# Performance work log

Measured on AMD Instinct MI355X. Metric: run time of the kernel, lower is better.

The kernel has to match this reference:

```python
import jax, jax.numpy as jnp
import numpy as np

B, E, H, W, L = 16, 32, 512, 512, 3  # batch, emb channels, height, width, n classes (bg/plant/disease)
MAX_NEIGHBOR = 3


def _per_image_loss(emb, pred, label, neighbor):
    """emb: (E,H,W) f32; pred: (L,H,W) f32 logits; label: (H,W) int32; neighbor: (L,MAX_NEIGHBOR) int32."""
    P = H * W
    emb_f = emb.reshape(E, P)                                      # (E,P)
    lab_f = label.reshape(P)
    onehot = (lab_f[None, :] == jnp.arange(L)[:, None]).astype(emb.dtype)  # (L,P)
    counts = onehot.sum(axis=1)                                    # (L,)

    # per-label mean embeddings (segment mean) and L2-normalized means (F.normalize eps=1e-12)
    means = (onehot @ emb_f.T) / counts[:, None]                   # (L,E)
    norm_means = means / jnp.maximum(jnp.linalg.norm(means, axis=1, keepdims=True), 1e-12)

    # intra loss: mean over masked pixels of (1 - cos(norm_mean, pixel)), labels 1..L-1
    pix_hat = emb_f / jnp.maximum(jnp.linalg.norm(emb_f, axis=0, keepdims=True), 1e-8)  # CosineSimilarity eps
    cos = norm_means @ pix_hat                                     # (L,P)
    intra_per = (onehot * (1.0 - cos)).sum(axis=1) / counts        # (L,)
    intra = intra_per[1:].sum() / (L - 1)

    # inter loss: pairwise cosine of normalized means, masked by neighbor table
    S = norm_means @ norm_means.T                                  # (L,L)
    # inter_mask: for main_label>=1, mark neighbor entries until first 0 (break semantics)
    valid = jnp.cumprod((neighbor != 0).astype(jnp.float32), axis=1)        # (L,MAX_NEIGHBOR)
    rows = jnp.broadcast_to(jnp.arange(L)[:, None], (L, MAX_NEIGHBOR))
    row_ok = (rows >= 1).astype(jnp.float32)
    mask = jnp.zeros((L, L), dtype=jnp.float32).at[
        rows.reshape(-1), neighbor.reshape(-1)
    ].max((valid * row_ok).reshape(-1))
    inter = (S * mask).sum() / mask.sum()

    # cross-entropy (labels in [0,L), ignore_index=255 never hit here), mean over pixels
    logp = jax.nn.log_softmax(pred, axis=0)                        # (L,H,W)
    ce = -jnp.take_along_axis(logp, label[None, :, :].astype(jnp.int32), axis=0).mean()

    return intra + inter + ce


def setup_inputs() -> dict:
    key = jax.random.key(0)
    k1, k2, k3 = jax.random.split(key, 3)
    embedding = jax.random.normal(k1, (B, E, H, W), dtype=jnp.float32)
    prediction = jax.random.normal(k2, (B, L, H, W), dtype=jnp.float32)
    class_label = jax.random.randint(k3, (B, H, W), 0, L).astype(jnp.int32)
    # realistic neighbor table: plant(1)<->disease(2) adjacent, 0 = terminator
    nb = np.tile(np.array([[0, 0, 0], [2, 0, 0], [1, 0, 0]], dtype=np.int32), (B, 1, 1))
    neighbor = jnp.asarray(nb)
    return {"embedding": embedding, "prediction": prediction,
            "class_label": class_label, "neighbor": neighbor}


def reference(embedding, prediction, class_label, neighbor):
    losses = jax.vmap(_per_image_loss)(embedding, prediction, class_label, neighbor)  # (B,)
    return losses.sum()
```

## Files before the change

kernel.cpp:

```cpp
#include <hip/hip_runtime.h>
#include <math.h>

#define BATCH 16
#define EMB   32
#define HW    262144
#define NL    3

#define BLOCKS_PER_IMG 128
#define PX_PER_BLOCK   (HW / BLOCKS_PER_IMG)
#define WAVES_PER_BLK  4
#define PX_PER_WAVE    (PX_PER_BLOCK / WAVES_PER_BLK)
#define TILE_PX        32
#define N_ITERS        (PX_PER_WAVE / TILE_PX)

#define WS_COUNTS 0
#define WS_SE     64
#define WS_SH     (WS_SE + BATCH*96)
#define WS_CE     (WS_SH + BATCH*96)
#define WS_FLOATS (WS_CE + 1)

__device__ __forceinline__ float ce1(float a, float b, float c, int l) {
    const float m = fmaxf(fmaxf(a, b), c);
    const float s = __expf(a - m) + __expf(b - m) + __expf(c - m);
    const float zl = (l == 0) ? a : ((l == 1) ? b : c);
    return m + __logf(s) - zl;
}

__global__ __launch_bounds__(256) void fused_kernel(
        const float* __restrict__ emb, const float* __restrict__ pred,
        const int* __restrict__ label, float* __restrict__ ws)
{
    const int tid  = threadIdx.x;
    const int lane = tid & 63;
    const int wv   = tid >> 6;
    const int ps   = lane & 7;
    const int cg   = lane >> 3;
    const int b    = blockIdx.x / BLOCKS_PER_IMG;
    const int blk  = blockIdx.x % BLOCKS_PER_IMG;

    const float* embB  = emb   + (size_t)b * EMB * HW;
    const float* predB = pred  + (size_t)b * 3 * HW;
    const int*   labB  = label + (size_t)b * HW;

    const size_t base = (size_t)blk * PX_PER_BLOCK
                      + (size_t)wv * PX_PER_WAVE
                      + (size_t)ps * 4;

    const float* ch0 = embB + (size_t)(cg*4+0)*HW + base;
    const float* ch1 = embB + (size_t)(cg*4+1)*HW + base;
    const float* ch2 = embB + (size_t)(cg*4+2)*HW + base;
    const float* ch3 = embB + (size_t)(cg*4+3)*HW + base;
    const int*   lb  = labB + base;
    const float* pr  = predB + base;

    float accE[NL][4] = {};
    float accH[2][4]  = {};
    float cnt0 = 0.f, cnt1 = 0.f, cnt2 = 0.f;
    float ce = 0.f;

    for (int it = 0; it < N_ITERS; ++it) {
        const size_t off = (size_t)it * TILE_PX;

        const float4 v0 = *(const float4*)(ch0 + off);
        const float4 v1 = *(const float4*)(ch1 + off);
        const float4 v2 = *(const float4*)(ch2 + off);
        const float4 v3 = *(const float4*)(ch3 + off);
        const int4  lab = *(const int4*)(lb + off);

        const bool doCE = (cg == (it & 7));
        float4 z0, z1, z2;
        if (doCE) {
            z0 = *(const float4*)(pr + off);
            z1 = *(const float4*)(pr + HW + off);
            z2 = *(const float4*)(pr + 2*HW + off);
        }

        float4 s;
        s.x = v0.x*v0.x + v1.x*v1.x + v2.x*v2.x + v3.x*v3.x;
        s.y = v0.y*v0.y + v1.y*v1.y + v2.y*v2.y + v3.y*v3.y;
        s.z = v0.z*v0.z + v1.z*v1.z + v2.z*v2.z + v3.z*v3.z;
        s.w = v0.w*v0.w + v1.w*v1.w + v2.w*v2.w + v3.w*v3.w;
        s.x += __shfl_xor(s.x, 8);  s.x += __shfl_xor(s.x, 16);  s.x += __shfl_xor(s.x, 32);
        s.y += __shfl_xor(s.y, 8);  s.y += __shfl_xor(s.y, 16);  s.y += __shfl_xor(s.y, 32);
        s.z += __shfl_xor(s.z, 8);  s.z += __shfl_xor(s.z, 16);  s.z += __shfl_xor(s.z, 32);
        s.w += __shfl_xor(s.w, 8);  s.w += __shfl_xor(s.w, 16);  s.w += __shfl_xor(s.w, 32);

        float invn[4];
        invn[0] = 1.0f / fmaxf(sqrtf(s.x), 1e-8f);
        invn[1] = 1.0f / fmaxf(sqrtf(s.y), 1e-8f);
        invn[2] = 1.0f / fmaxf(sqrtf(s.z), 1e-8f);
        invn[3] = 1.0f / fmaxf(sqrtf(s.w), 1e-8f);

        const float chv[4][4] = {
            {v0.x, v1.x, v2.x, v3.x},
            {v0.y, v1.y, v2.y, v3.y},
            {v0.z, v1.z, v2.z, v3.z},
            {v0.w, v1.w, v2.w, v3.w}};
        const int labs[4] = {lab.x, lab.y, lab.z, lab.w};

        #pragma unroll
        for (int j = 0; j < 4; ++j) {
            const float m0 = (labs[j] == 0) ? 1.f : 0.f;
            const float m1 = (labs[j] == 1) ? 1.f : 0.f;
            const float m2 = (labs[j] == 2) ? 1.f : 0.f;
            const float iv = invn[j];
            if (cg == 0) { cnt0 += m0; cnt1 += m1; cnt2 += m2; }
            #pragma unroll
            for (int k = 0; k < 4; ++k) {
                const float v  = chv[j][k];
                const float vh = v * iv;
                accE[0][k] = fmaf(m0, v,  accE[0][k]);
                accE[1][k] = fmaf(m1, v,  accE[1][k]);
                accE[2][k] = fmaf(m2, v,  accE[2][k]);
                accH[0][k] = fmaf(m1, vh, accH[0][k]);
                accH[1][k] = fmaf(m2, vh, accH[1][k]);
            }
        }

        if (doCE) {
            ce += ce1(z0.x, z1.x, z2.x, labs[0]);
            ce += ce1(z0.y, z1.y, z2.y, labs[1]);
            ce += ce1(z0.z, z1.z, z2.z, labs[2]);
            ce += ce1(z0.w, z1.w, z2.w, labs[3]);
        }
    }

    #pragma unroll
    for (int o = 4; o >= 1; o >>= 1) {
        #pragma unroll
        for (int l = 0; l < NL; ++l)
            #pragma unroll
            for (int k = 0; k < 4; ++k)
                accE[l][k] += __shfl_xor(accE[l][k], o);
        #pragma unroll
        for (int l = 0; l < 2; ++l)
            #pragma unroll
            for (int k = 0; k < 4; ++k)
                accH[l][k] += __shfl_xor(accH[l][k], o);
        cnt0 += __shfl_xor(cnt0, o);
        cnt1 += __shfl_xor(cnt1, o);
        cnt2 += __shfl_xor(cnt2, o);
    }
    #pragma unroll
    for (int o = 32; o >= 1; o >>= 1) ce += __shfl_xor(ce, o);

    if (ps == 0) {
        float* se = ws + WS_SE + b * 96;
        float* sh = ws + WS_SH + b * 96;
        #pragma unroll
        for (int l = 0; l < NL; ++l)
            #pragma unroll
            for (int k = 0; k < 4; ++k)
                atomicAdd(&se[l*32 + cg*4 + k], accE[l][k]);
        #pragma unroll
        for (int l = 0; l < 2; ++l)
            #pragma unroll
            for (int k = 0; k < 4; ++k)
                atomicAdd(&sh[(l+1)*32 + cg*4 + k], accH[l][k]);
    }
    if (lane == 0) {
        atomicAdd(&ws[WS_CE], ce * (1.0f / (float)HW));
        atomicAdd(&ws[WS_COUNTS + b*4 + 0], cnt0);
        atomicAdd(&ws[WS_COUNTS + b*4 + 1], cnt1);
        atomicAdd(&ws[WS_COUNTS + b*4 + 2], cnt2);
    }
}

__global__ __launch_bounds__(512) void final_kernel(
        const int* __restrict__ nbr, const float* __restrict__ ws,
        float* __restrict__ out)
{
    const int tid = threadIdx.x;
    const int b = tid >> 5;
    const int e = tid & 31;
    __shared__ float total;
    if (tid == 0) total = 0.f;
    __syncthreads();

    const float* se = ws + WS_SE + b * 96;
    const float* sh = ws + WS_SH + b * 96;
    const float c0 = ws[WS_COUNTS + b*4 + 0];
    const float c1 = ws[WS_COUNTS + b*4 + 1];
    const float c2 = ws[WS_COUNTS + b*4 + 2];

    float mean0 = se[0*32 + e] / c0;
    float mean1 = se[1*32 + e] / c1;
    float mean2 = se[2*32 + e] / c2;

    float n0 = mean0*mean0, n1 = mean1*mean1, n2 = mean2*mean2;
    #pragma unroll
    for (int o = 16; o >= 1; o >>= 1) {
        n0 += __shfl_xor(n0, o);
        n1 += __shfl_xor(n1, o);
        n2 += __shfl_xor(n2, o);
    }
    const float nm0 = mean0 / fmaxf(sqrtf(n0), 1e-12f);
    const float nm1 = mean1 / fmaxf(sqrtf(n1), 1e-12f);
    const float nm2 = mean2 / fmaxf(sqrtf(n2), 1e-12f);

    float d1  = nm1 * sh[1*32 + e];
    float d2  = nm2 * sh[2*32 + e];
    float s10 = nm1 * nm0, s11 = nm1 * nm1, s12 = nm1 * nm2;
    float s20 = nm2 * nm0, s21 = nm2 * nm1, s22 = nm2 * nm2;
    #pragma unroll
    for (int o = 16; o >= 1; o >>= 1) {
        d1  += __shfl_xor(d1, o);  d2  += __shfl_xor(d2, o);
        s10 += __shfl_xor(s10, o); s11 += __shfl_xor(s11, o); s12 += __shfl_xor(s12, o);
        s20 += __shfl_xor(s20, o); s21 += __shfl_xor(s21, o); s22 += __shfl_xor(s22, o);
    }

    if (e == 0) {
        float S[3][3];
        S[1][0] = s10; S[1][1] = s11; S[1][2] = s12;
        S[2][0] = s20; S[2][1] = s21; S[2][2] = s22;
        S[0][0] = S[0][1] = S[0][2] = 0.f;
        float mask[3][3] = {{0.f,0.f,0.f},{0.f,0.f,0.f},{0.f,0.f,0.f}};
        for (int row = 1; row < 3; ++row) {
            int prod = 1;
            for (int j = 0; j < 3; ++j) {
                const int v = nbr[b*9 + row*3 + j];
                if (v == 0) prod = 0;
                if (prod) mask[row][v] = 1.f;
            }
        }
        float num = 0.f, den = 0.f;
        for (int row = 1; row < 3; ++row)
            for (int col = 0; col < 3; ++col) {
                num += S[row][col] * mask[row][col];
                den += mask[row][col];
            }
        const float inter = num / den;
        const float ip1 = 1.f - d1 / c1;
        const float ip2 = 1.f - d2 / c2;
        const float loss = 0.5f * (ip1 + ip2) + inter;
        atomicAdd(&total, loss);
    }
    __syncthreads();
    if (tid == 0) out[0] = total + ws[WS_CE];
}

extern "C" void kernel_launch(void* const* d_in, const int* in_sizes, int n_in,
                              void* d_out, int out_size, void* d_ws, size_t ws_size,
                              hipStream_t stream) {
    const float* emb   = (const float*)d_in[0];
    const float* pred  = (const float*)d_in[1];
    const int*   label = (const int*)d_in[2];
    const int*   nbr   = (const int*)d_in[3];
    float* ws  = (float*)d_ws;
    float* out = (float*)d_out;

    hipMemsetAsync(d_ws, 0, WS_FLOATS * sizeof(float), stream);
    fused_kernel<<<BATCH * BLOCKS_PER_IMG, 256, 0, stream>>>(emb, pred, label, ws);
    final_kernel<<<1, 512, 0, stream>>>(nbr, ws, out);
}
```

Baseline: 864.7 us.

## Stage embedding tiles in LDS, one 256-pixel tile per block

Replaces the per-wave streaming loop with one 256-pixel tile per block. The block loads all 32 channels into a padded shared-memory tile and computes pixel norms through a shared partial-sum buffer. The transposed tile is then reduced per channel group, which removes the per-pixel cross-lane shuffles for norms and spreads the cross-entropy work evenly across threads. The cost is eight times more blocks and roughly twice as many global atomics onto the same few per-image addresses. The float4 stores into rows with an odd stride of 257 floats may also be misaligned.

```diff
diff --git a/kernel.cpp b/kernel.cpp
--- a/kernel.cpp
+++ b/kernel.cpp
@@ -6,12 +6,8 @@
 #define HW    262144
 #define NL    3
 
-#define BLOCKS_PER_IMG 128
-#define PX_PER_BLOCK   (HW / BLOCKS_PER_IMG)
-#define WAVES_PER_BLK  4
-#define PX_PER_WAVE    (PX_PER_BLOCK / WAVES_PER_BLK)
-#define TILE_PX        32
-#define N_ITERS        (PX_PER_WAVE / TILE_PX)
+#define TILE_PX        256
+#define TILES_PER_IMG  (HW / TILE_PX)
 
 #define WS_COUNTS 0
 #define WS_SE     64
@@ -30,113 +26,90 @@
         const float* __restrict__ emb, const float* __restrict__ pred,
         const int* __restrict__ label, float* __restrict__ ws)
 {
-    const int tid  = threadIdx.x;
-    const int lane = tid & 63;
-    const int wv   = tid >> 6;
-    const int ps   = lane & 7;
-    const int cg   = lane >> 3;
-    const int b    = blockIdx.x / BLOCKS_PER_IMG;
-    const int blk  = blockIdx.x % BLOCKS_PER_IMG;
-
-    const float* embB  = emb   + (size_t)b * EMB * HW;
-    const float* predB = pred  + (size_t)b * 3 * HW;
-    const int*   labB  = label + (size_t)b * HW;
-
-    const size_t base = (size_t)blk * PX_PER_BLOCK
-                      + (size_t)wv * PX_PER_WAVE
-                      + (size_t)ps * 4;
-
-    const float* ch0 = embB + (size_t)(cg*4+0)*HW + base;
-    const float* ch1 = embB + (size_t)(cg*4+1)*HW + base;
-    const float* ch2 = embB + (size_t)(cg*4+2)*HW + base;
-    const float* ch3 = embB + (size_t)(cg*4+3)*HW + base;
-    const int*   lb  = labB + base;
-    const float* pr  = predB + base;
+    const int tid = threadIdx.x;
+    const int wv  = tid >> 6;
+    const int l   = tid & 63;
+    const int b   = blockIdx.x >> 10;
+    const int t0  = (blockIdx.x & 1023) * TILE_PX;
+
+    const float* embB  = emb   + (size_t)b * EMB * HW + t0;
+    const float* predB = pred  + (size_t)b * 3 * HW + t0;
+    const int*   labB  = label + (size_t)b * HW + t0;
+
+    __shared__ float embT[32][TILE_PX + 1];
+    __shared__ float partF[4][TILE_PX];
+    __shared__ float invnL[TILE_PX];
+    __shared__ int   labL[TILE_PX];
+
+    float4 ps4 = {0.f, 0.f, 0.f, 0.f};
+    #pragma unroll
+    for (int i = 0; i < 8; ++i) {
+        const int c = wv * 8 + i;
+        const float4 v = *(const float4*)(embB + (size_t)c * HW + l * 4);
+        ps4.x = fmaf(v.x, v.x, ps4.x);
+        ps4.y = fmaf(v.y, v.y, ps4.y);
+        ps4.z = fmaf(v.z, v.z, ps4.z);
+        ps4.w = fmaf(v.w, v.w, ps4.w);
+        *(float4*)&embT[c][l * 4] = v;
+    }
+    *(float4*)&partF[wv][l * 4] = ps4;
+    if (wv == 0) {
+        const int4 lb4 = *(const int4*)(labB + l * 4);
+        *(int4*)&labL[l * 4] = lb4;
+    }
+    __syncthreads();
+
+    const float ss = partF[0][tid] + partF[1][tid] + partF[2][tid] + partF[3][tid];
+    const float iv = 1.0f / fmaxf(sqrtf(ss), 1e-8f);
+    invnL[tid] = iv;
+    const int lbp = labL[tid];
+    const float z0 = predB[tid];
+    const float z1 = predB[HW + tid];
+    const float z2 = predB[2 * HW + tid];
+    float ce = ce1(z0, z1, z2, lbp);
+    __syncthreads();
+
+    const int cg = tid >> 5;
+    const int pl = tid & 31;
+    const int c0 = cg * 4;
 
     float accE[NL][4] = {};
     float accH[2][4]  = {};
     float cnt0 = 0.f, cnt1 = 0.f, cnt2 = 0.f;
-    float ce = 0.f;
-
-    for (int it = 0; it < N_ITERS; ++it) {
-        const size_t off = (size_t)it * TILE_PX;
-
-        const float4 v0 = *(const float4*)(ch0 + off);
-        const float4 v1 = *(const float4*)(ch1 + off);
-        const float4 v2 = *(const float4*)(ch2 + off);
-        const float4 v3 = *(const float4*)(ch3 + off);
-        const int4  lab = *(const int4*)(lb + off);
-
-        const bool doCE = (cg == (it & 7));
-        float4 z0, z1, z2;
-        if (doCE) {
-            z0 = *(const float4*)(pr + off);
-            z1 = *(const float4*)(pr + HW + off);
-            z2 = *(const float4*)(pr + 2*HW + off);
+
+    #pragma unroll
+    for (int s = 0; s < 8; ++s) {
+        const int p = pl + 32 * s;
+        const int lb = labL[p];
+        const float ivp = invnL[p];
+        const float m0 = (lb == 0) ? 1.f : 0.f;
+        const float m1 = (lb == 1) ? 1.f : 0.f;
+        const float m2 = (lb == 2) ? 1.f : 0.f;
+        if (cg == 0) { cnt0 += m0; cnt1 += m1; cnt2 += m2; }
+        #pragma unroll
+        for (int k = 0; k < 4; ++k) {
+            const float v  = embT[c0 + k][p];
+            const float vh = v * ivp;
+            accE[0][k] = fmaf(m0, v,  accE[0][k]);
+            accE[1][k] = fmaf(m1, v,  accE[1][k]);
+            accE[2][k] = fmaf(m2, v,  accE[2][k]);
+            accH[0][k] = fmaf(m1, vh, accH[0][k]);
+            accH[1][k] = fmaf(m2, vh, accH[1][k]);
         }
-
-        float4 s;
-        s.x = v0.x*v0.x + v1.x*v1.x + v2.x*v2.x + v3.x*v3.x;
-        s.y = v0.y*v0.y + v1.y*v1.y + v2.y*v2.y + v3.y*v3.y;
-        s.z = v0.z*v0.z + v1.z*v1.z + v2.z*v2.z + v3.z*v3.z;
-        s.w = v0.w*v0.w + v1.w*v1.w + v2.w*v2.w + v3.w*v3.w;
-        s.x += __shfl_xor(s.x, 8);  s.x += __shfl_xor(s.x, 16);  s.x += __shfl_xor(s.x, 32);
-        s.y += __shfl_xor(s.y, 8);  s.y += __shfl_xor(s.y, 16);  s.y += __shfl_xor(s.y, 32);
-        s.z += __shfl_xor(s.z, 8);  s.z += __shfl_xor(s.z, 16);  s.z += __shfl_xor(s.z, 32);
-        s.w += __shfl_xor(s.w, 8);  s.w += __shfl_xor(s.w, 16);  s.w += __shfl_xor(s.w, 32);
-
-        float invn[4];
-        invn[0] = 1.0f / fmaxf(sqrtf(s.x), 1e-8f);
-        invn[1] = 1.0f / fmaxf(sqrtf(s.y), 1e-8f);
-        invn[2] = 1.0f / fmaxf(sqrtf(s.z), 1e-8f);
-        invn[3] = 1.0f / fmaxf(sqrtf(s.w), 1e-8f);
-
-        const float chv[4][4] = {
-            {v0.x, v1.x, v2.x, v3.x},
-            {v0.y, v1.y, v2.y, v3.y},
-            {v0.z, v1.z, v2.z, v3.z},
-            {v0.w, v1.w, v2.w, v3.w}};
-        const int labs[4] = {lab.x, lab.y, lab.z, lab.w};
-
-        #pragma unroll
-        for (int j = 0; j < 4; ++j) {
-            const float m0 = (labs[j] == 0) ? 1.f : 0.f;
-            const float m1 = (labs[j] == 1) ? 1.f : 0.f;
-            const float m2 = (labs[j] == 2) ? 1.f : 0.f;
-            const float iv = invn[j];
-            if (cg == 0) { cnt0 += m0; cnt1 += m1; cnt2 += m2; }
-            #pragma unroll
-            for (int k = 0; k < 4; ++k) {
-                const float v  = chv[j][k];
-                const float vh = v * iv;
-                accE[0][k] = fmaf(m0, v,  accE[0][k]);
-                accE[1][k] = fmaf(m1, v,  accE[1][k]);
-                accE[2][k] = fmaf(m2, v,  accE[2][k]);
-                accH[0][k] = fmaf(m1, vh, accH[0][k]);
-                accH[1][k] = fmaf(m2, vh, accH[1][k]);
-            }
-        }
-
-        if (doCE) {
-            ce += ce1(z0.x, z1.x, z2.x, labs[0]);
-            ce += ce1(z0.y, z1.y, z2.y, labs[1]);
-            ce += ce1(z0.z, z1.z, z2.z, labs[2]);
-            ce += ce1(z0.w, z1.w, z2.w, labs[3]);
-        }
-    }
-
-    #pragma unroll
-    for (int o = 4; o >= 1; o >>= 1) {
-        #pragma unroll
-        for (int l = 0; l < NL; ++l)
-            #pragma unroll
-            for (int k = 0; k < 4; ++k)
-                accE[l][k] += __shfl_xor(accE[l][k], o);
-        #pragma unroll
-        for (int l = 0; l < 2; ++l)
-            #pragma unroll
-            for (int k = 0; k < 4; ++k)
-                accH[l][k] += __shfl_xor(accH[l][k], o);
+    }
+
+    #pragma unroll
+    for (int o = 16; o >= 1; o >>= 1) {
+        #pragma unroll
+        for (int ll = 0; ll < NL; ++ll)
+            #pragma unroll
+            for (int k = 0; k < 4; ++k)
+                accE[ll][k] += __shfl_xor(accE[ll][k], o);
+        #pragma unroll
+        for (int ll = 0; ll < 2; ++ll)
+            #pragma unroll
+            for (int k = 0; k < 4; ++k)
+                accH[ll][k] += __shfl_xor(accH[ll][k], o);
         cnt0 += __shfl_xor(cnt0, o);
         cnt1 += __shfl_xor(cnt1, o);
         cnt2 += __shfl_xor(cnt2, o);
@@ -144,22 +117,22 @@
     #pragma unroll
     for (int o = 32; o >= 1; o >>= 1) ce += __shfl_xor(ce, o);
 
-    if (ps == 0) {
+    if (pl == 0) {
         float* se = ws + WS_SE + b * 96;
         float* sh = ws + WS_SH + b * 96;
         #pragma unroll
-        for (int l = 0; l < NL; ++l)
-            #pragma unroll
-            for (int k = 0; k < 4; ++k)
-                atomicAdd(&se[l*32 + cg*4 + k], accE[l][k]);
-        #pragma unroll
-        for (int l = 0; l < 2; ++l)
-            #pragma unroll
-            for (int k = 0; k < 4; ++k)
-                atomicAdd(&sh[(l+1)*32 + cg*4 + k], accH[l][k]);
-    }
-    if (lane == 0) {
-        atomicAdd(&ws[WS_CE], ce * (1.0f / (float)HW));
+        for (int ll = 0; ll < NL; ++ll)
+            #pragma unroll
+            for (int k = 0; k < 4; ++k)
+                atomicAdd(&se[ll*32 + c0 + k], accE[ll][k]);
+        #pragma unroll
+        for (int ll = 0; ll < 2; ++ll)
+            #pragma unroll
+            for (int k = 0; k < 4; ++k)
+                atomicAdd(&sh[(ll+1)*32 + c0 + k], accH[ll][k]);
+    }
+    if (l == 0) atomicAdd(&ws[WS_CE], ce * (1.0f / (float)HW));
+    if (tid == 0) {
         atomicAdd(&ws[WS_COUNTS + b*4 + 0], cnt0);
         atomicAdd(&ws[WS_COUNTS + b*4 + 1], cnt1);
         atomicAdd(&ws[WS_COUNTS + b*4 + 2], cnt2);
@@ -250,6 +223,6 @@
     float* out = (float*)d_out;
 
     hipMemsetAsync(d_ws, 0, WS_FLOATS * sizeof(float), stream);
-    fused_kernel<<<BATCH * BLOCKS_PER_IMG, 256, 0, stream>>>(emb, pred, label, ws);
+    fused_kernel<<<BATCH * TILES_PER_IMG, 256, 0, stream>>>(emb, pred, label, ws);
     final_kernel<<<1, 512, 0, stream>>>(nbr, ws, out);
 }
```

New measurement: 1.568 ms. 81.4% more time.
